# Kernel optimization log

Hardware: AMD Instinct MI355X
Metric: run time of the kernel (lower is better)

## Reference

```python
import jax, jax.numpy as jnp
import numpy as np

D_MODEL = 1024
NUM_HEADS = 16
D_K = D_MODEL // NUM_HEADS
BASE = 10000.0


def _rope_tables(seq_len, d_model, dtype):
    # positions start at 1 (torch.arange(1, seq_len+1)), theta over d_model (full width!)
    pos = jnp.arange(1, seq_len + 1, dtype=dtype)[:, None]            # (S, 1)
    theta = BASE ** (-2.0 * jnp.arange(d_model // 2, dtype=dtype) / d_model)  # (D/2,)
    m_theta = pos * theta                                              # (S, D/2)
    return jnp.cos(m_theta), jnp.sin(m_theta)


def _rotate_half(x):
    d = x.shape[-1]
    return jnp.concatenate([-x[..., d // 2:], x[..., :d // 2]], axis=-1)


def _apply_rope(x):
    # x: (B, S, D). Module applies RoPE on full d_model before projections,
    # inside @torch.no_grad() -> stop_gradient for faithfulness.
    S, D = x.shape[1], x.shape[2]
    cos, sin = _rope_tables(S, D, x.dtype)
    cos_ri = jnp.repeat(cos, 2, axis=-1)  # interleaved repeat, (S, D)
    sin_ri = jnp.repeat(sin, 2, axis=-1)
    return jax.lax.stop_gradient(x * cos_ri + _rotate_half(x) * sin_ri)


def setup_inputs() -> dict:
    key = jax.random.key(0)
    ks = jax.random.split(key, 11)
    B, S, D = 2, 2048, D_MODEL
    scale = 1.0 / np.sqrt(D)
    return {
        "q": jax.random.normal(ks[0], (B, S, D), jnp.float32),
        "k": jax.random.normal(ks[1], (B, S, D), jnp.float32),
        "v": jax.random.normal(ks[2], (B, S, D), jnp.float32),
        "Wq_w": jax.random.normal(ks[3], (D, D), jnp.float32) * scale,
        "Wq_b": jnp.zeros((D,), jnp.float32),
        "Wk_w": jax.random.normal(ks[4], (D, D), jnp.float32) * scale,
        "Wk_b": jnp.zeros((D,), jnp.float32),
        "Wv_w": jax.random.normal(ks[5], (D, D), jnp.float32) * scale,
        "Wv_b": jnp.zeros((D,), jnp.float32),
        "Wo_w": jax.random.normal(ks[6], (D, D), jnp.float32) * scale,
        "Wo_b": jnp.zeros((D,), jnp.float32),
    }


def reference(q, k, v, Wq_w, Wq_b, Wk_w, Wk_b, Wv_w, Wv_b, Wo_w, Wo_b):
    B, S, D = q.shape
    q = _apply_rope(q)
    k = _apply_rope(k)
    # projections (torch Linear: x @ W.T + b)
    def split_heads(x):
        return x.reshape(B, S, NUM_HEADS, D_K).transpose(0, 2, 1, 3)  # (B, H, S, d_k)
    Q = split_heads(q @ Wq_w.T + Wq_b)
    K = split_heads(k @ Wk_w.T + Wk_b)
    V = split_heads(v @ Wv_w.T + Wv_b)
    scores = jnp.einsum("bhqd,bhkd->bhqk", Q, K) / jnp.sqrt(jnp.float32(D_K))
    attn = jax.nn.softmax(scores, axis=-1)
    out = jnp.einsum("bhqk,bhkd->bhqd", attn, V)       # (B, H, S, d_k)
    out = out.transpose(0, 2, 1, 3).reshape(B, S, D)   # concat heads
    return out @ Wo_w.T + Wo_b
```

## Files before the change

### kernel.cpp

```cpp
#include <hip/hip_runtime.h>
#include <hip/hip_bf16.h>
#include <cstdint>

#define B_  2
#define S_  2048
#define D_  1024
#define H_  16
#define DK_ 64

typedef unsigned short u16;
typedef __attribute__((ext_vector_type(8))) __bf16 bf16x8;
typedef __attribute__((ext_vector_type(4))) float  f32x4;

__device__ __forceinline__ u16 f2bf(float f) {
  union { float f; uint32_t u; } x; x.f = f;
  uint32_t r = (x.u + 0x7fffu + ((x.u >> 16) & 1u)) >> 16;
  return (u16)r;
}

__device__ __forceinline__ uint32_t cvt_pk_bf16(float lo, float hi) {
  uint32_t r;
  asm volatile("v_cvt_pk_bf16_f32 %0, %1, %2" : "=v"(r) : "v"(lo), "v"(hi));
  return r;
}

__device__ __forceinline__ void gload_lds16(const void* g, void* l) {
  __builtin_amdgcn_global_load_lds(
      (const __attribute__((address_space(1))) void*)g,
      (__attribute__((address_space(3))) void*)l, 16, 0, 0);
}

__global__ __launch_bounds__(256) void rope_tables_k(float* __restrict__ cosT,
                                                     float* __restrict__ sinT) {
  int idx = blockIdx.x * 256 + threadIdx.x;
  int s = idx >> 9;
  int i = idx & 511;
  double theta = exp((-2.0 * (double)i / (double)D_) * log(10000.0));
  double arg = (double)(s + 1) * theta;
  cosT[idx] = (float)cos(arg);
  sinT[idx] = (float)sin(arg);
}

__global__ __launch_bounds__(256) void rope_apply(
    const float* __restrict__ q, const float* __restrict__ k, const float* __restrict__ v,
    const float* __restrict__ cosT, const float* __restrict__ sinT,
    u16* __restrict__ qr, u16* __restrict__ kr, u16* __restrict__ vb) {
  const int row = blockIdx.x;
  const int j   = threadIdx.x;
  const int s   = row & (S_ - 1);
  const float c0 = cosT[s * 512 + j],       s0 = sinT[s * 512 + j];
  const float c1 = cosT[s * 512 + 256 + j], s1 = sinT[s * 512 + 256 + j];
  const size_t off = (size_t)row * D_;

  float2 qa = *(const float2*)(q + off + 2 * j);
  float2 qb = *(const float2*)(q + off + 2 * j + 512);
  qr[off + 2*j]       = f2bf(qa.x * c0 - qb.x * s0);
  qr[off + 2*j + 1]   = f2bf(qa.y * c0 - qb.y * s0);
  qr[off + 2*j + 512] = f2bf(qb.x * c1 + qa.x * s1);
  qr[off + 2*j + 513] = f2bf(qb.y * c1 + qa.y * s1);

  float2 ka = *(const float2*)(k + off + 2 * j);
  float2 kb = *(const float2*)(k + off + 2 * j + 512);
  kr[off + 2*j]       = f2bf(ka.x * c0 - kb.x * s0);
  kr[off + 2*j + 1]   = f2bf(ka.y * c0 - kb.y * s0);
  kr[off + 2*j + 512] = f2bf(kb.x * c1 + ka.x * s1);
  kr[off + 2*j + 513] = f2bf(kb.y * c1 + ka.y * s1);

  float2 va = *(const float2*)(v + off + 2 * j);
  float2 vv = *(const float2*)(v + off + 2 * j + 512);
  vb[off + 2*j]       = f2bf(va.x);
  vb[off + 2*j + 1]   = f2bf(va.y);
  vb[off + 2*j + 512] = f2bf(vv.x);
  vb[off + 2*j + 513] = f2bf(vv.y);
}

__global__ __launch_bounds__(256) void cvt4_k(const float* __restrict__ w0,
                                              const float* __restrict__ w1,
                                              const float* __restrict__ w2,
                                              const float* __restrict__ w3,
                                              u16* __restrict__ out) {
  int i = (blockIdx.x * 256 + threadIdx.x) * 4;
  int which = i >> 20;
  const float* src = which == 0 ? w0 : which == 1 ? w1 : which == 2 ? w2 : w3;
  float4 f = *(const float4*)(src + (i & 1048575));
  out[i]     = f2bf(f.x);
  out[i + 1] = f2bf(f.y);
  out[i + 2] = f2bf(f.z);
  out[i + 3] = f2bf(f.w);
}

template <int MODE>
__global__ __launch_bounds__(256) void gemm_bt(
    const u16* __restrict__ A, const u16* __restrict__ W,
    const float* __restrict__ bias, void* __restrict__ out,
    int M, int N, int K) {
  __shared__ __align__(16) u16 At[2][128 * 64];
  __shared__ __align__(16) u16 Bt[2][128 * 64];
  const int lane = threadIdx.x & 63;
  const int wv   = threadIdx.x >> 6;
  const int wm   = wv >> 1, wn = wv & 1;
  const int nT   = N / 128;
  const int tileM = (blockIdx.x / nT) * 128;
  const int tileN = (blockIdx.x % nT) * 128;
  const int lr = lane & 15;
  const int g  = lane >> 4;
  const int lk = g * 8;

  f32x4 acc[4][4];
#pragma unroll
  for (int i = 0; i < 4; ++i)
#pragma unroll
    for (int j = 0; j < 4; ++j) acc[i][j] = (f32x4){0.f, 0.f, 0.f, 0.f};

#define GSTAGE(buf, kbn) do {                                                  \
    _Pragma("unroll")                                                          \
    for (int r2 = 0; r2 < 4; ++r2) {                                           \
      int c = r2 * 256 + wv * 64 + lane;                                       \
      int row = c >> 3;                                                        \
      int scol = (((c & 7) * 16) ^ ((row & 7) << 4)) >> 1;                     \
      gload_lds16(A + (size_t)(tileM + row) * K + (kbn) + scol,                \
                  (void*)(At[buf] + (r2 * 256 + wv * 64) * 8));                \
      gload_lds16(W + (size_t)(tileN + row) * K + (kbn) + scol,                \
                  (void*)(Bt[buf] + (r2 * 256 + wv * 64) * 8));                \
    }                                                                          \
  } while (0)

  GSTAGE(0, 0);
  __syncthreads();
  for (int kb = 0; kb < K; kb += 64) {
    const int cur = (kb >> 6) & 1;
    if (kb + 64 < K) GSTAGE(cur ^ 1, kb + 64);
#pragma unroll
    for (int kk = 0; kk < 2; ++kk) {
      const int sw = ((kk * 64 + g * 16) ^ ((lr & 7) << 4)) >> 1;
      bf16x8 af[4], bfr[4];
#pragma unroll
      for (int i = 0; i < 4; ++i)
        af[i] = *(const bf16x8*)(At[cur] + (wm * 64 + i * 16 + lr) * 64 + sw);
#pragma unroll
      for (int i = 0; i < 4; ++i)
        bfr[i] = *(const bf16x8*)(Bt[cur] + (wn * 64 + i * 16 + lr) * 64 + sw);
#pragma unroll
      for (int mi = 0; mi < 4; ++mi)
#pragma unroll
        for (int ni = 0; ni < 4; ++ni)
          acc[mi][ni] = __builtin_amdgcn_mfma_f32_16x16x32_bf16(af[mi], bfr[ni],
                                                                acc[mi][ni], 0, 0, 0);
    }
    __syncthreads();
  }
#undef GSTAGE

#pragma unroll
  for (int mi = 0; mi < 4; ++mi)
#pragma unroll
    for (int ni = 0; ni < 4; ++ni)
#pragma unroll
      for (int r = 0; r < 4; ++r) {
        int m = tileM + wm * 64 + mi * 16 + g * 4 + r;
        int n = tileN + wn * 64 + ni * 16 + lr;
        float val = acc[mi][ni][r] + bias[n];
        if (MODE == 2) {
          ((float*)out)[(size_t)m * N + n] = val;
        } else {
          int bb = m >> 11, ss = m & (S_ - 1);
          int hh = n >> 6, dk = n & 63;
          if (MODE == 0)
            ((u16*)out)[(((size_t)(bb * H_ + hh) * S_ + ss) << 6) + dk] = f2bf(val);
          else
            ((u16*)out)[(((size_t)(bb * H_ + hh) * DK_ + dk) << 11) + ss] = f2bf(val);
        }
      }
}

__global__ __launch_bounds__(256, 2) void attn_kernel(
    const u16* __restrict__ Qh, const u16* __restrict__ Kh,
    const u16* __restrict__ Vt, u16* __restrict__ Oout) {
  __shared__ __align__(16) u16 Kt[2][64 * 64];
  __shared__ __align__(16) u16 Plds[4][32 * 72];
  const int lane = threadIdx.x & 63;
  const int wv   = threadIdx.x >> 6;
  const int lr = lane & 15, g = lane >> 4, lk = g * 8;
  const int swzm = (lr & 3) << 4;
  const int sw = (blockIdx.x & 7) * 64 + (blockIdx.x >> 3);
  const int bh = sw >> 4;
  const int qb = (sw & 15) * 128;
  const int b = bh >> 4, h = bh & 15;
  const size_t base = (size_t)bh * S_ * DK_;
  const int qrow = qb + wv * 32;
  u16* Pw = &Plds[wv][0];

  bf16x8 qf[2][2];
#pragma unroll
  for (int m = 0; m < 2; ++m)
#pragma unroll
    for (int i = 0; i < 2; ++i)
      qf[m][i] = *(const bf16x8*)(Qh + base + (size_t)(qrow + m * 16 + lr) * DK_ + i * 32 + lk);

  f32x4 acc[2][4];
  f32x4 lsum[2];
#pragma unroll
  for (int m = 0; m < 2; ++m) {
    lsum[m] = (f32x4){0.f, 0.f, 0.f, 0.f};
#pragma unroll
    for (int n = 0; n < 4; ++n) acc[m][n] = (f32x4){0.f, 0.f, 0.f, 0.f};
  }

  const float C1 = 0.18033688f;
  const float C2 = 11.54156036f;

#define STAGE_K(nb, kbn) do {                                                  \
    _Pragma("unroll")                                                          \
    for (int r2 = 0; r2 < 2; ++r2) {                                           \
      int c = r2 * 256 + wv * 64 + lane;                                       \
      int row = c >> 3;                                                        \
      int scol = (((c & 7) * 16) ^ ((row & 7) << 4)) >> 1;                     \
      gload_lds16(Kh + base + (size_t)((kbn) + row) * DK_ + scol,              \
                  (void*)(Kt[nb] + (r2 * 256 + wv * 64) * 8));                 \
    }                                                                          \
  } while (0)

  STAGE_K(0, 0);
  __syncthreads();

  for (int kb = 0; kb < S_; kb += 64) {
    const int cur = (kb >> 6) & 1;
    if (kb + 64 < S_) STAGE_K(cur ^ 1, kb + 64);
    bf16x8 vf[2][4];
#pragma unroll
    for (int ks = 0; ks < 2; ++ks)
#pragma unroll
      for (int n = 0; n < 4; ++n)
        vf[ks][n] = *(const bf16x8*)(Vt + ((size_t)bh * DK_ + n * 16 + lr) * S_
                                     + kb + ks * 32 + lk);
    bf16x8 kf[4][2];
#pragma unroll
    for (int f = 0; f < 4; ++f)
#pragma unroll
      for (int half = 0; half < 2; ++half) {
        const int swk = ((half * 64 + g * 16) ^ ((lr & 7) << 4)) >> 1;
        kf[f][half] = *(const bf16x8*)(Kt[cur] + (f * 16 + lr) * 64 + swk);
      }
    f32x4 sc[4][2];
#pragma unroll
    for (int f = 0; f < 4; ++f) {
      sc[f][0] = (f32x4){0.f, 0.f, 0.f, 0.f};
      sc[f][1] = (f32x4){0.f, 0.f, 0.f, 0.f};
    }
#pragma unroll
    for (int f = 0; f < 4; ++f) {
      sc[f][0] = __builtin_amdgcn_mfma_f32_16x16x32_bf16(kf[f][0], qf[0][0], sc[f][0], 0, 0, 0);
      sc[f][0] = __builtin_amdgcn_mfma_f32_16x16x32_bf16(kf[f][1], qf[0][1], sc[f][0], 0, 0, 0);
      sc[f][1] = __builtin_amdgcn_mfma_f32_16x16x32_bf16(kf[f][0], qf[1][0], sc[f][1], 0, 0, 0);
      sc[f][1] = __builtin_amdgcn_mfma_f32_16x16x32_bf16(kf[f][1], qf[1][1], sc[f][1], 0, 0, 0);
    }
#pragma unroll
    for (int m = 0; m < 2; ++m) {
      const int row = m * 16 + lr;
#pragma unroll
      for (int f = 0; f < 4; ++f) {
        f32x4 p;
        p[0] = __builtin_amdgcn_exp2f(fmaf(sc[f][m][0], C1, -C2));
        p[1] = __builtin_amdgcn_exp2f(fmaf(sc[f][m][1], C1, -C2));
        p[2] = __builtin_amdgcn_exp2f(fmaf(sc[f][m][2], C1, -C2));
        p[3] = __builtin_amdgcn_exp2f(fmaf(sc[f][m][3], C1, -C2));
        lsum[m] += p;
        uint2 w;
        w.x = cvt_pk_bf16(p[0], p[1]);
        w.y = cvt_pk_bf16(p[2], p[3]);
        *(uint2*)(Pw + row * 72 + ((f * 16 + g * 4) ^ swzm)) = w;
      }
    }
    bf16x8 pa[2][2];
#pragma unroll
    for (int m = 0; m < 2; ++m)
#pragma unroll
      for (int ks = 0; ks < 2; ++ks)
        pa[m][ks] = *(const bf16x8*)(Pw + (m * 16 + lr) * 72 + ((ks * 32 + lk) ^ swzm));
#pragma unroll
    for (int ks = 0; ks < 2; ++ks)
#pragma unroll
      for (int n = 0; n < 4; ++n) {
        acc[0][n] = __builtin_amdgcn_mfma_f32_16x16x32_bf16(pa[0][ks], vf[ks][n], acc[0][n], 0, 0, 0);
        acc[1][n] = __builtin_amdgcn_mfma_f32_16x16x32_bf16(pa[1][ks], vf[ks][n], acc[1][n], 0, 0, 0);
      }
    __syncthreads();
  }
#undef STAGE_K

#pragma unroll
  for (int m = 0; m < 2; ++m) {
    float s = lsum[m][0] + lsum[m][1] + lsum[m][2] + lsum[m][3];
    s += __shfl_xor(s, 16);
    s += __shfl_xor(s, 32);
#pragma unroll
    for (int r = 0; r < 4; ++r) {
      float inv = 1.0f / __shfl(s, g * 4 + r);
      int row = b * S_ + qrow + m * 16 + g * 4 + r;
#pragma unroll
      for (int n = 0; n < 4; ++n)
        Oout[(size_t)row * D_ + h * 64 + n * 16 + lr] = f2bf(acc[m][n][r] * inv);
    }
  }
}

extern "C" void kernel_launch(void* const* d_in, const int* in_sizes, int n_in,
                              void* d_out, int out_size, void* d_ws, size_t ws_size,
                              hipStream_t stream) {
  const float* q    = (const float*)d_in[0];
  const float* k    = (const float*)d_in[1];
  const float* v    = (const float*)d_in[2];
  const float* Wq_w = (const float*)d_in[3];
  const float* Wq_b = (const float*)d_in[4];
  const float* Wk_w = (const float*)d_in[5];
  const float* Wk_b = (const float*)d_in[6];
  const float* Wv_w = (const float*)d_in[7];
  const float* Wv_b = (const float*)d_in[8];
  const float* Wo_w = (const float*)d_in[9];
  const float* Wo_b = (const float*)d_in[10];

  char* ws = (char*)d_ws;
  const size_t MB = 1024 * 1024;
  float* cosT = (float*)(ws);
  float* sinT = (float*)(ws + 4 * MB);
  u16* qr  = (u16*)(ws + 8 * MB);
  u16* kr  = (u16*)(ws + 16 * MB);
  u16* vb  = (u16*)(ws + 24 * MB);
  u16* Wqh = (u16*)(ws + 32 * MB);
  u16* Wkh = (u16*)(ws + 34 * MB);
  u16* Wvh = (u16*)(ws + 36 * MB);
  u16* Woh = (u16*)(ws + 38 * MB);
  u16* Qh  = (u16*)(ws);
  u16* Kh  = (u16*)(ws + 8 * MB);
  u16* Vt  = (u16*)(ws + 16 * MB);
  u16* attn_o = (u16*)(ws + 24 * MB);

  rope_tables_k<<<dim3(S_ * 512 / 256), dim3(256), 0, stream>>>(cosT, sinT);
  rope_apply<<<dim3(B_ * S_), dim3(256), 0, stream>>>(q, k, v, cosT, sinT, qr, kr, vb);

  cvt4_k<<<dim3(4 * D_ * D_ / 4 / 256), dim3(256), 0, stream>>>(Wq_w, Wk_w, Wv_w, Wo_w, Wqh);

  const int M = B_ * S_, N = D_, K = D_;
  dim3 ggrid((M / 128) * (N / 128));
  gemm_bt<0><<<ggrid, dim3(256), 0, stream>>>(qr, Wqh, Wq_b, (void*)Qh, M, N, K);
  gemm_bt<0><<<ggrid, dim3(256), 0, stream>>>(kr, Wkh, Wk_b, (void*)Kh, M, N, K);
  gemm_bt<1><<<ggrid, dim3(256), 0, stream>>>(vb, Wvh, Wv_b, (void*)Vt, M, N, K);

  attn_kernel<<<dim3(B_ * H_ * (S_ / 128)), dim3(256), 0, stream>>>(Qh, Kh, Vt, attn_o);

  gemm_bt<2><<<ggrid, dim3(256), 0, stream>>>(attn_o, Woh, Wo_b, d_out, M, N, K);
}
```

Before: 288.3 us.

## Shrink GEMM tiles to 128x64 with BK=32 and swizzled block order

The projection GEMMs now use 128x64 output tiles with a K-step of 32 instead of 128x128 with K-step 64. This doubles the grid to 512 blocks so the device's compute units are filled better, and it adds an XOR-swizzled LDS layout plus an L2-friendly block remap. The template mode parameter becomes a runtime argument. In exchange there is less reuse per tile, twice as many barriers per K step, and a runtime branch in the epilogue.

```diff
diff --git a/kernel.cpp b/kernel.cpp
--- a/kernel.cpp
+++ b/kernel.cpp
@@ -89,64 +89,68 @@
   out[i + 3] = f2bf(f.w);
 }
 
-template <int MODE>
-__global__ __launch_bounds__(256) void gemm_bt(
+__global__ __launch_bounds__(256) void gemm_bt2(
     const u16* __restrict__ A, const u16* __restrict__ W,
     const float* __restrict__ bias, void* __restrict__ out,
-    int M, int N, int K) {
-  __shared__ __align__(16) u16 At[2][128 * 64];
-  __shared__ __align__(16) u16 Bt[2][128 * 64];
-  const int lane = threadIdx.x & 63;
-  const int wv   = threadIdx.x >> 6;
+    int M, int N, int K, int mode) {
+  __shared__ __align__(16) u16 At[2][128 * 32];
+  __shared__ __align__(16) u16 Bt[2][64 * 32];
+  const int tid  = threadIdx.x;
+  const int lane = tid & 63;
+  const int wv   = tid >> 6;
   const int wm   = wv >> 1, wn = wv & 1;
-  const int nT   = N / 128;
-  const int tileM = (blockIdx.x / nT) * 128;
-  const int tileN = (blockIdx.x % nT) * 128;
+  const int sw = (blockIdx.x & 7) * 64 + (blockIdx.x >> 3);
+  const int tileM = (sw >> 4) * 128;
+  const int tileN = (sw & 15) * 64;
   const int lr = lane & 15;
   const int g  = lane >> 4;
-  const int lk = g * 8;
-
-  f32x4 acc[4][4];
+
+  f32x4 acc[4][2];
 #pragma unroll
   for (int i = 0; i < 4; ++i)
 #pragma unroll
-    for (int j = 0; j < 4; ++j) acc[i][j] = (f32x4){0.f, 0.f, 0.f, 0.f};
+    for (int j = 0; j < 2; ++j) acc[i][j] = (f32x4){0.f, 0.f, 0.f, 0.f};
 
 #define GSTAGE(buf, kbn) do {                                                  \
     _Pragma("unroll")                                                          \
-    for (int r2 = 0; r2 < 4; ++r2) {                                           \
-      int c = r2 * 256 + wv * 64 + lane;                                       \
-      int row = c >> 3;                                                        \
-      int scol = (((c & 7) * 16) ^ ((row & 7) << 4)) >> 1;                     \
-      gload_lds16(A + (size_t)(tileM + row) * K + (kbn) + scol,                \
+    for (int r2 = 0; r2 < 2; ++r2) {                                           \
+      int c = r2 * 256 + tid;                                                  \
+      int row = c >> 2;                                                        \
+      int sch = ((c & 3) ^ ((row >> 1) & 3)) * 8;                              \
+      gload_lds16(A + (size_t)(tileM + row) * K + (kbn) + sch,                 \
                   (void*)(At[buf] + (r2 * 256 + wv * 64) * 8));                \
-      gload_lds16(W + (size_t)(tileN + row) * K + (kbn) + scol,                \
-                  (void*)(Bt[buf] + (r2 * 256 + wv * 64) * 8));                \
+    }                                                                          \
+    {                                                                          \
+      int c = tid;                                                             \
+      int row = c >> 2;                                                        \
+      int sch = ((c & 3) ^ ((row >> 1) & 3)) * 8;                              \
+      gload_lds16(W + (size_t)(tileN + row) * K + (kbn) + sch,                 \
+                  (void*)(Bt[buf] + (wv * 64) * 8));                           \
     }                                                                          \
   } while (0)
 
   GSTAGE(0, 0);
   __syncthreads();
-  for (int kb = 0; kb < K; kb += 64) {
-    const int cur = (kb >> 6) & 1;
-    if (kb + 64 < K) GSTAGE(cur ^ 1, kb + 64);
-#pragma unroll
-    for (int kk = 0; kk < 2; ++kk) {
-      const int sw = ((kk * 64 + g * 16) ^ ((lr & 7) << 4)) >> 1;
-      bf16x8 af[4], bfr[4];
-#pragma unroll
-      for (int i = 0; i < 4; ++i)
-        af[i] = *(const bf16x8*)(At[cur] + (wm * 64 + i * 16 + lr) * 64 + sw);
-#pragma unroll
-      for (int i = 0; i < 4; ++i)
-        bfr[i] = *(const bf16x8*)(Bt[cur] + (wn * 64 + i * 16 + lr) * 64 + sw);
-#pragma unroll
-      for (int mi = 0; mi < 4; ++mi)
-#pragma unroll
-        for (int ni = 0; ni < 4; ++ni)
-          acc[mi][ni] = __builtin_amdgcn_mfma_f32_16x16x32_bf16(af[mi], bfr[ni],
-                                                                acc[mi][ni], 0, 0, 0);
-    }
+  for (int kb = 0; kb < K; kb += 32) {
+    const int cur = (kb >> 5) & 1;
+    if (kb + 32 < K) GSTAGE(cur ^ 1, kb + 32);
+    bf16x8 af[4], bfr[2];
+#pragma unroll
+    for (int i = 0; i < 4; ++i) {
+      int r = wm * 64 + i * 16 + lr;
+      af[i] = *(const bf16x8*)(At[cur] + r * 32 + (g ^ ((r >> 1) & 3)) * 8);
+    }
+#pragma unroll
+    for (int i = 0; i < 2; ++i) {
+      int r = wn * 32 + i * 16 + lr;
+      bfr[i] = *(const bf16x8*)(Bt[cur] + r * 32 + (g ^ ((r >> 1) & 3)) * 8);
+    }
+#pragma unroll
+    for (int mi = 0; mi < 4; ++mi)
+#pragma unroll
+      for (int ni = 0; ni < 2; ++ni)
+        acc[mi][ni] = __builtin_amdgcn_mfma_f32_16x16x32_bf16(af[mi], bfr[ni],
+                                                              acc[mi][ni], 0, 0, 0);
     __syncthreads();
   }
 #undef GSTAGE
@@ -154,18 +158,18 @@
 #pragma unroll
   for (int mi = 0; mi < 4; ++mi)
 #pragma unroll
-    for (int ni = 0; ni < 4; ++ni)
+    for (int ni = 0; ni < 2; ++ni)
 #pragma unroll
       for (int r = 0; r < 4; ++r) {
         int m = tileM + wm * 64 + mi * 16 + g * 4 + r;
-        int n = tileN + wn * 64 + ni * 16 + lr;
+        int n = tileN + wn * 32 + ni * 16 + lr;
         float val = acc[mi][ni][r] + bias[n];
-        if (MODE == 2) {
+        if (mode == 2) {
           ((float*)out)[(size_t)m * N + n] = val;
         } else {
           int bb = m >> 11, ss = m & (S_ - 1);
           int hh = n >> 6, dk = n & 63;
-          if (MODE == 0)
+          if (mode == 0)
             ((u16*)out)[(((size_t)(bb * H_ + hh) * S_ + ss) << 6) + dk] = f2bf(val);
           else
             ((u16*)out)[(((size_t)(bb * H_ + hh) * DK_ + dk) << 11) + ss] = f2bf(val);
@@ -341,12 +345,12 @@
   cvt4_k<<<dim3(4 * D_ * D_ / 4 / 256), dim3(256), 0, stream>>>(Wq_w, Wk_w, Wv_w, Wo_w, Wqh);
 
   const int M = B_ * S_, N = D_, K = D_;
-  dim3 ggrid((M / 128) * (N / 128));
-  gemm_bt<0><<<ggrid, dim3(256), 0, stream>>>(qr, Wqh, Wq_b, (void*)Qh, M, N, K);
-  gemm_bt<0><<<ggrid, dim3(256), 0, stream>>>(kr, Wkh, Wk_b, (void*)Kh, M, N, K);
-  gemm_bt<1><<<ggrid, dim3(256), 0, stream>>>(vb, Wvh, Wv_b, (void*)Vt, M, N, K);
+  dim3 ggrid((M / 128) * (N / 64));
+  gemm_bt2<<<ggrid, dim3(256), 0, stream>>>(qr, Wqh, Wq_b, (void*)Qh, M, N, K, 0);
+  gemm_bt2<<<ggrid, dim3(256), 0, stream>>>(kr, Wkh, Wk_b, (void*)Kh, M, N, K, 0);
+  gemm_bt2<<<ggrid, dim3(256), 0, stream>>>(vb, Wvh, Wv_b, (void*)Vt, M, N, K, 1);
 
   attn_kernel<<<dim3(B_ * H_ * (S_ / 128)), dim3(256), 0, stream>>>(Qh, Kh, Vt, attn_o);
 
-  gemm_bt<2><<<ggrid, dim3(256), 0, stream>>>(attn_o, Woh, Wo_b, d_out, M, N, K);
-}
+  gemm_bt2<<<ggrid, dim3(256), 0, stream>>>(attn_o, Woh, Wo_b, d_out, M, N, K, 2);
+}
```

Result: no change. 290.5 us (+0.8%).
